# Kernel tuning notes

Measured on AMD Instinct MI355X. Metric: run time of the kernel, lower is better.

Reference implementation:

```python
import jax, jax.numpy as jnp
import numpy as np

KS = 3      # kernel_size
PAD = 1     # padding
STRIDE = 1
B, C_IN, C_OUT, H, W = 4, 64, 128, 128, 128


def _conv(x, w, stride, padding):
    return jax.lax.conv_general_dilated(
        x, w, (stride, stride), padding,
        dimension_numbers=("NCHW", "OIHW", "NCHW"))


def setup_inputs() -> dict:
    key = jax.random.key(0)
    k1, k2, k3, k4 = jax.random.split(key, 4)
    N = KS * KS
    x = jax.random.normal(k1, (B, C_IN, H, W), jnp.float32)
    # offset conv: Conv2d(inc, 2*ks*ks, 3, padding=1, stride=1). (Original inits
    # weight to 0; we use small random weights so the bilinear gather is exercised.)
    w_off = jax.random.normal(k2, (2 * N, C_IN, 3, 3), jnp.float32) * 0.01
    b_off = jax.random.normal(k3, (2 * N,), jnp.float32) * 0.01
    # main conv: Conv2d(inc, outc, ks, stride=ks, bias=False)
    w_conv = jax.random.normal(k4, (C_OUT, C_IN, KS, KS), jnp.float32) / np.sqrt(C_IN * KS * KS)
    return {"x": x, "w_off": w_off, "b_off": b_off, "w_conv": w_conv}


def deform_forward(x, w_off, b_off, w_conv):
    ks, pad, stride = KS, PAD, STRIDE
    N = ks * ks
    offset = _conv(x, w_off, stride, [(1, 1), (1, 1)]) + b_off[None, :, None, None]
    b, _, h, w = offset.shape
    xp = jnp.pad(x, ((0, 0), (0, 0), (pad, pad), (pad, pad)))
    Hp, Wp = xp.shape[2], xp.shape[3]

    # p_n: relative kernel offsets, layout [y coords (N), x coords (N)]
    r = jnp.arange(-(ks - 1) // 2, (ks - 1) // 2 + 1)
    pny, pnx = jnp.meshgrid(r, r, indexing="ij")
    p_n = jnp.concatenate([pny.ravel(), pnx.ravel()]).astype(offset.dtype).reshape(1, 2 * N, 1, 1)

    # p_0: absolute output-pixel centers (1-based due to zero padding)
    p0y, p0x = jnp.meshgrid(jnp.arange(1, h * stride + 1, stride),
                            jnp.arange(1, w * stride + 1, stride), indexing="ij")
    p_0 = jnp.concatenate([jnp.tile(p0y[None, None], (1, N, 1, 1)),
                           jnp.tile(p0x[None, None], (1, N, 1, 1))], axis=1).astype(offset.dtype)

    p = (p_0 + p_n + offset).transpose(0, 2, 3, 1)  # (b, h, w, 2N)

    # four integer corners (indices are non-differentiable / detached)
    q_lt_f = jnp.floor(jax.lax.stop_gradient(p))
    q_rb_f = q_lt_f + 1

    def clamp_yx(q):
        return jnp.concatenate([jnp.clip(q[..., :N], 0, Hp - 1),
                                jnp.clip(q[..., N:], 0, Wp - 1)], axis=-1).astype(jnp.int32)

    q_lt = clamp_yx(q_lt_f)
    q_rb = clamp_yx(q_rb_f)
    q_lb = jnp.concatenate([q_lt[..., :N], q_rb[..., N:]], axis=-1)
    q_rt = jnp.concatenate([q_rb[..., :N], q_lt[..., N:]], axis=-1)

    # points falling in the padding region snap to floor(p)
    mask = jnp.concatenate([
        (p[..., :N] < pad) | (p[..., :N] > Hp - 1 - pad),
        (p[..., N:] < pad) | (p[..., N:] > Wp - 1 - pad)], axis=-1).astype(p.dtype)
    mask = jax.lax.stop_gradient(mask)
    floor_p = jnp.floor(p)
    p = p * (1 - mask) + floor_p * mask
    p = jnp.concatenate([jnp.clip(p[..., :N], 0, Hp - 1),
                         jnp.clip(p[..., N:], 0, Wp - 1)], axis=-1)

    f = lambda q: q.astype(p.dtype)
    g_lt = (1 + (f(q_lt[..., :N]) - p[..., :N])) * (1 + (f(q_lt[..., N:]) - p[..., N:]))
    g_rb = (1 - (f(q_rb[..., :N]) - p[..., :N])) * (1 - (f(q_rb[..., N:]) - p[..., N:]))
    g_lb = (1 + (f(q_lb[..., :N]) - p[..., :N])) * (1 - (f(q_lb[..., N:]) - p[..., N:]))
    g_rt = (1 - (f(q_rt[..., :N]) - p[..., :N])) * (1 + (f(q_rt[..., N:]) - p[..., N:]))

    c = xp.shape[1]
    x_flat = xp.reshape(b, c, Hp * Wp)  # (b, c, Hp*Wp)

    def get_x_q(q):
        idx = (q[..., :N] * Wp + q[..., N:]).reshape(b, 1, h * w * N)
        return jnp.take_along_axis(x_flat, idx, axis=2).reshape(b, c, h, w, N)

    x_off = (g_lt[:, None] * get_x_q(q_lt) + g_rb[:, None] * get_x_q(q_rb)
             + g_lb[:, None] * get_x_q(q_lb) + g_rt[:, None] * get_x_q(q_rt))

    # (b, c, h, w, N=ks*ks) -> (b, c, h*ks, w*ks): sample n maps to kernel cell (n//ks, n%ks)
    x_off = x_off.reshape(b, c, h, w, ks, ks).transpose(0, 1, 2, 4, 3, 5).reshape(b, c, h * ks, w * ks)

    return _conv(x_off, w_conv, ks, "VALID")  # stride=ks, no bias


def reference(x, w_off, b_off, w_conv):
    return deform_forward(x, w_off, b_off, w_conv)
```

## Files before the change

### kernel.cpp

```cpp
#include <hip/hip_runtime.h>
#include <hip/hip_fp16.h>

#define NB 4
#define CI 64
#define CO 128
#define HH 128
#define WW 128
#define HWSZ (HH*WW)
#define TOTPX (NB*HWSZ)
#define NN 9

using half8 = __attribute__((ext_vector_type(8))) _Float16;
using f32x4 = __attribute__((ext_vector_type(4))) float;
using f32x2 = __attribute__((ext_vector_type(2))) float;

__global__ __launch_bounds__(256) void k_prep_w(const float* __restrict__ w,
                                                unsigned short* __restrict__ waF,
                                                const float* __restrict__ w_off,
                                                float* __restrict__ wP) {
    int t = blockIdx.x * 256 + threadIdx.x;
    if (t < CO * 576) {
        int oc = t / 576, r = t - oc * 576;
        int c = r / 9, n = r - c * 9;
        int i = oc >> 4, col = oc & 15;
        int ks = c >> 5, koct = (c >> 3) & 3, e = c & 7;
        int lane = koct * 16 + col;
        waF[(n * 16 + i * 2 + ks) * 512 + lane * 8 + e] =
            __half_as_ushort(__float2half_rn(w[t]));
    }
    if (t < 18 * 576) {
        int oc = t / 576, r = t - oc * 576;
        wP[r * 20 + oc] = w_off[t];
    }
}

__global__ __launch_bounds__(512, 8) void k_offsets(
    const float* __restrict__ x, const float* __restrict__ wP,
    const float* __restrict__ b_off, uchar4* __restrict__ dC,
    ushort4* __restrict__ dG, unsigned short* __restrict__ xT)
{
    __shared__ f32x2 sm[512 * 9];
    int bid = blockIdx.x;
    int b = bid >> 8, rem = bid & 255, y = rem >> 1, x0 = (rem & 1) << 6;
    int t = threadIdx.x;
    int pxl = t & 63;
    int g   = __builtin_amdgcn_readfirstlane(t >> 6);
    int xg = x0 + pxl;

    f32x2 a2[9];
    #pragma unroll
    for (int i = 0; i < 9; i++) a2[i] = {0.f, 0.f};

    #pragma unroll 2
    for (int ci = 0; ci < 8; ci++) {
        int cg = g * 8 + ci;
        const float* xpl = x + (size_t)(b * CI + cg) * HWSZ;
        #pragma unroll
        for (int ky = 0; ky < 3; ky++) {
            int yy = y + ky - 1;
            if ((unsigned)yy >= 128u) continue;
            const float* xr = xpl + yy * WW;
            #pragma unroll
            for (int kx = 0; kx < 3; kx++) {
                int xx = xg + kx - 1;
                float v = ((unsigned)xx < 128u) ? xr[xx] : 0.f;
                const f32x2* wr2 = (const f32x2*)(wP + (cg * 9 + ky * 3 + kx) * 20);
                f32x2 v2 = {v, v};
                #pragma unroll
                for (int j = 0; j < 9; j++)
                    a2[j] = __builtin_elementwise_fma(v2, wr2[j], a2[j]);
            }
        }
    }

    {
        const float* xc = x + ((size_t)(b * CI + g * 8) * HH + y) * WW + xg;
        unsigned short c8[8];
        #pragma unroll
        for (int ci = 0; ci < 8; ci++)
            c8[ci] = __half_as_ushort(__float2half_rn(xc[(size_t)ci * HWSZ]));
        size_t pbase = (size_t)((b * HH + y) * WW + xg) * 64 + g * 8;
        *(uint4*)(xT + pbase) = *(const uint4*)&c8[0];
    }

    #pragma unroll
    for (int i = 0; i < 9; i++) sm[t * 9 + i] = a2[i];
    __syncthreads();

    for (int task = t; task < 576; task += 512) {
        int p2 = task & 63, n = task >> 6;
        float ay = b_off[n], ax = b_off[9 + n];
        int jy = n >> 1, cy = n & 1;
        int jx = (9 + n) >> 1, cx = (9 + n) & 1;
        #pragma unroll
        for (int gg = 0; gg < 8; gg++) {
            ay += sm[(gg * 64 + p2) * 9 + jy][cy];
            ax += sm[(gg * 64 + p2) * 9 + jx][cx];
        }
        float py  = (float)(y + (n / 3)) + ay;
        float pxc = (float)(x0 + p2 + (n % 3)) + ax;
        float fy = floorf(py), fx = floorf(pxc);
        if (py  < 1.f || py  > 128.f) py  = fy;
        if (pxc < 1.f || pxc > 128.f) pxc = fx;
        py  = fminf(fmaxf(py,  0.f), 129.f);
        pxc = fminf(fmaxf(pxc, 0.f), 129.f);

        fy = floorf(py); fx = floorf(pxc);
        int y0 = (int)fy, x0i = (int)fx;
        int y1 = min(y0 + 1, 129), x1 = min(x0i + 1, 129);
        float wyl = 1.f + (fy - py);
        float wyr = 1.f - ((float)y1 - py);
        float wxl = 1.f + (fx - pxc);
        float wxr = 1.f - ((float)x1 - pxc);
        float glt = wyl * wxl, grb = wyr * wxr, glb = wyl * wxr, grt = wyr * wxl;
        if ((unsigned)(y0  - 1) >= 128u) { glt = 0.f; glb = 0.f; }
        if ((unsigned)(y1  - 1) >= 128u) { grb = 0.f; grt = 0.f; }
        if ((unsigned)(x0i - 1) >= 128u) { glt = 0.f; grt = 0.f; }
        if ((unsigned)(x1  - 1) >= 128u) { grb = 0.f; glb = 0.f; }

        uchar4 cu;
        cu.x = (unsigned char)min(max(y0  - 1, 0), 127);
        cu.y = (unsigned char)min(max(y1  - 1, 0), 127);
        cu.z = (unsigned char)min(max(x0i - 1, 0), 127);
        cu.w = (unsigned char)min(max(x1  - 1, 0), 127);
        ushort4 gu;
        gu.x = __half_as_ushort(__float2half_rn(glt));
        gu.y = __half_as_ushort(__float2half_rn(grb));
        gu.z = __half_as_ushort(__float2half_rn(glb));
        gu.w = __half_as_ushort(__float2half_rn(grt));
        int pixIdx = (b * HH + y) * WW + x0 + p2;
        dC[n * TOTPX + pixIdx] = cu;
        dG[n * TOTPX + pixIdx] = gu;
    }
}

__global__ __launch_bounds__(256, 4) void k_main(
    const unsigned short* __restrict__ xT, const unsigned short* __restrict__ waF,
    const uchar4* __restrict__ dC, const ushort4* __restrict__ dG,
    float* __restrict__ out)
{
    __shared__ __align__(16) unsigned short Wl[2][8192];
    __shared__ __align__(16) unsigned short Rd[4][1024];

    int bid0 = blockIdx.x;
    int bid  = ((bid0 & 7) << 7) | (bid0 >> 3);
    int b = bid >> 8, rem = bid & 255, y = rem >> 1, x0 = (rem & 1) << 6;

    int t = threadIdx.x, lane = t & 63, wv = t >> 6;
    int col = lane & 15, koct = lane >> 4;
    int gp = lane >> 2, gq = lane & 3;
    int qo = gq * 8;
    int pixG = (b * HH + y) * WW + x0 + wv * 16 + gp;
    const unsigned short* xb = xT + (size_t)b * (HWSZ * 64);

    half8 raw[8];
    f32x4 acc[8];
    #pragma unroll
    for (int i = 0; i < 8; i++) acc[i] = {0.f, 0.f, 0.f, 0.f};

    auto stage = [&](int kc, int buf) {
        #pragma unroll
        for (int p = 0; p < 4; p++) {
            const unsigned short* gsrc = waF + kc * 8192 + wv * 512 + p * 2048 + lane * 8;
            __builtin_amdgcn_global_load_lds(
                (const __attribute__((address_space(1))) unsigned int*)gsrc,
                (__attribute__((address_space(3))) unsigned int*)&Wl[buf][wv * 512 + p * 2048],
                16, 0, 0);
        }
    };
    auto issue = [&](uchar4 cu) {
        int o00 = (((int)cu.x * WW) + (int)cu.z) << 6;
        int o11 = (((int)cu.y * WW) + (int)cu.w) << 6;
        int o01 = (((int)cu.x * WW) + (int)cu.w) << 6;
        int o10 = (((int)cu.y * WW) + (int)cu.z) << 6;
        raw[0] = *(const half8*)(xb + o00 + qo);
        raw[1] = *(const half8*)(xb + o11 + qo);
        raw[2] = *(const half8*)(xb + o01 + qo);
        raw[3] = *(const half8*)(xb + o10 + qo);
        raw[4] = *(const half8*)(xb + o00 + qo + 32);
        raw[5] = *(const half8*)(xb + o11 + qo + 32);
        raw[6] = *(const half8*)(xb + o01 + qo + 32);
        raw[7] = *(const half8*)(xb + o10 + qo + 32);
    };
    auto combine_store = [&](ushort4 gu) {
        __half2 q0 = __half2half2(__ushort_as_half(gu.x));
        __half2 q1 = __half2half2(__ushort_as_half(gu.y));
        __half2 q2 = __half2half2(__ushort_as_half(gu.z));
        __half2 q3 = __half2half2(__ushort_as_half(gu.w));
        #pragma unroll
        for (int ks = 0; ks < 2; ks++) {
            __half2 vm[4];
            #pragma unroll
            for (int m = 0; m < 4; m++) {
                __half2 v = __hmul2(((const __half2*)&raw[ks * 4 + 0])[m], q0);
                v = __hfma2(((const __half2*)&raw[ks * 4 + 1])[m], q1, v);
                v = __hfma2(((const __half2*)&raw[ks * 4 + 2])[m], q2, v);
                v = __hfma2(((const __half2*)&raw[ks * 4 + 3])[m], q3, v);
                vm[m] = v;
            }
            int gz = (4 * ks + gq) ^ (gp & 7);
            *(uint4*)(&Rd[wv][0] + gp * 64 + gz * 8) = *(const uint4*)vm;
        }
    };

    stage(0, 0);
    __builtin_amdgcn_sched_barrier(0);
    uchar4  cuA = dC[pixG];          ushort4 guA = dG[pixG];
    uchar4  cuB = dC[TOTPX + pixG];  ushort4 guB = dG[TOTPX + pixG];
    __builtin_amdgcn_sched_barrier(0);
    issue(cuA);
    __builtin_amdgcn_sched_barrier(0);
    asm volatile("s_waitcnt vmcnt(8)" ::: "memory");
    __builtin_amdgcn_s_barrier();
    __builtin_amdgcn_sched_barrier(0);

#define ITER(KC)                                                              \
  {                                                                           \
    if ((KC) < 8) stage((KC) + 1, ((KC) & 1) ^ 1);                            \
    __builtin_amdgcn_sched_barrier(0);                                        \
    uchar4 cuN; ushort4 guN;                                                  \
    if ((KC) < 7) { cuN = dC[((KC)+2) * TOTPX + pixG];                        \
                    guN = dG[((KC)+2) * TOTPX + pixG]; }                      \
    __builtin_amdgcn_sched_barrier(0);                                        \
    combine_store(guA);                                                       \
    asm volatile("s_waitcnt lgkmcnt(0)" ::: "memory");                        \
    __builtin_amdgcn_sched_barrier(0);                                        \
    half8 bfr[2];                                                             \
    _Pragma("unroll")                                                         \
    for (int ks = 0; ks < 2; ks++) {                                          \
      int gz = (4 * ks + koct) ^ (col & 7);                                   \
      bfr[ks] = *(const half8*)(&Rd[wv][0] + col * 64 + gz * 8);              \
    }                                                                         \
    __builtin_amdgcn_sched_barrier(0);                                        \
    if ((KC) < 8) issue(cuB);                                                 \
    __builtin_amdgcn_sched_barrier(0);                                        \
    __builtin_amdgcn_s_setprio(1);                                            \
    { const unsigned short* wl = &Wl[(KC) & 1][0];                            \
      _Pragma("unroll")                                                       \
      for (int ks = 0; ks < 2; ks++)                                          \
        _Pragma("unroll")                                                     \
        for (int i = 0; i < 8; i++) {                                         \
          half8 af = *(const half8*)(wl + (i * 2 + ks) * 512 + lane * 8);     \
          acc[i] = __builtin_amdgcn_mfma_f32_16x16x32_f16(af, bfr[ks],        \
                                                          acc[i], 0, 0, 0); } } \
    __builtin_amdgcn_s_setprio(0);                                            \
    if ((KC) < 8) {                                                           \
      if ((KC) < 7) asm volatile("s_waitcnt vmcnt(10)" ::: "memory");         \
      else          asm volatile("s_waitcnt vmcnt(8)"  ::: "memory");         \
      __builtin_amdgcn_s_barrier();                                           \
      __builtin_amdgcn_sched_barrier(0);                                      \
    }                                                                         \
    cuA = cuB; guA = guB;                                                     \
    cuB = ((KC) < 7) ? cuN : cuB; guB = ((KC) < 7) ? guN : guB;               \
  }

    ITER(0) ITER(1) ITER(2) ITER(3) ITER(4) ITER(5) ITER(6) ITER(7) ITER(8)
#undef ITER

    int ob0 = b * CO * HWSZ + y * WW + x0 + wv * 16 + col;
    #pragma unroll
    for (int i = 0; i < 8; i++)
        #pragma unroll
        for (int r = 0; r < 4; r++) {
            int oc = i * 16 + koct * 4 + r;
            out[ob0 + oc * HWSZ] = acc[i][r];
        }
}

extern "C" void kernel_launch(void* const* d_in, const int* in_sizes, int n_in,
                              void* d_out, int out_size, void* d_ws, size_t ws_size,
                              hipStream_t stream) {
    const float* x      = (const float*)d_in[0];
    const float* w_off  = (const float*)d_in[1];
    const float* b_off  = (const float*)d_in[2];
    const float* w_conv = (const float*)d_in[3];
    float* out = (float*)d_out;

    char* wsb = (char*)d_ws;
    unsigned short* xT  = (unsigned short*)wsb;
    uchar4*         dC  = (uchar4*)(wsb + (size_t)TOTPX * 64 * 2);
    ushort4*        dG  = (ushort4*)(wsb + (size_t)TOTPX * 64 * 2 + (size_t)NN * TOTPX * 4);
    unsigned short* waF = (unsigned short*)(wsb + (size_t)TOTPX * 64 * 2
                                            + (size_t)NN * TOTPX * 4 + (size_t)NN * TOTPX * 8);
    float*          wP  = (float*)(wsb + (size_t)TOTPX * 64 * 2
                                   + (size_t)NN * TOTPX * 4 + (size_t)NN * TOTPX * 8
                                   + (size_t)CO * 576 * 2);

    k_prep_w<<<(CO * 576 + 255) / 256, 256, 0, stream>>>(w_conv, waF, w_off, wP);
    k_offsets<<<1024, 512, 0, stream>>>(x, wP, b_off, dC, dG, xT);
    k_main<<<1024, 256, 0, stream>>>(xT, waF, dC, dG, out);
}
```

Baseline: 58.39 us.

## Fuse offset computation into main deformable conv kernel, split NHWC transpose

The offset convolution and bilinear-coefficient computation now run inside the main MFMA kernel, one block per image row of 128 pixels and 512 threads. Coordinates and weights stay in LDS rather than going to global dC/dG arrays. The fp16 NHWC transpose of x moves to a separate LDS-tiled kernel, because the fused kernel gathers neighbouring pixels from other rows and so needs the whole transposed image first. This removes the global round-trip for offsets but adds a launch, halves the block count to 512, and makes the MFMA phase wait on the scalar offset conv inside each block.

```diff
diff --git a/kernel.cpp b/kernel.cpp
--- a/kernel.cpp
+++ b/kernel.cpp
@@ -34,71 +34,91 @@
     }
 }
 
-__global__ __launch_bounds__(512, 8) void k_offsets(
-    const float* __restrict__ x, const float* __restrict__ wP,
-    const float* __restrict__ b_off, uchar4* __restrict__ dC,
-    ushort4* __restrict__ dG, unsigned short* __restrict__ xT)
-{
-    __shared__ f32x2 sm[512 * 9];
+__global__ __launch_bounds__(256) void k_nhwc(const float* __restrict__ x,
+                                              unsigned short* __restrict__ xT) {
+    __shared__ float tl[64 * 65];
     int bid = blockIdx.x;
     int b = bid >> 8, rem = bid & 255, y = rem >> 1, x0 = (rem & 1) << 6;
     int t = threadIdx.x;
-    int pxl = t & 63;
-    int g   = __builtin_amdgcn_readfirstlane(t >> 6);
-    int xg = x0 + pxl;
-
-    f32x2 a2[9];
-    #pragma unroll
-    for (int i = 0; i < 9; i++) a2[i] = {0.f, 0.f};
-
-    #pragma unroll 2
-    for (int ci = 0; ci < 8; ci++) {
-        int cg = g * 8 + ci;
-        const float* xpl = x + (size_t)(b * CI + cg) * HWSZ;
-        #pragma unroll
-        for (int ky = 0; ky < 3; ky++) {
-            int yy = y + ky - 1;
-            if ((unsigned)yy >= 128u) continue;
-            const float* xr = xpl + yy * WW;
+    #pragma unroll
+    for (int i = 0; i < 16; i++) {
+        int idx = t + i * 256;
+        int c = idx >> 6, xl = idx & 63;
+        tl[c * 65 + xl] = x[((size_t)(b * CI + c) * HH + y) * WW + x0 + xl];
+    }
+    __syncthreads();
+    #pragma unroll
+    for (int i = 0; i < 16; i++) {
+        int idx = t + i * 256;
+        int xl = idx >> 6, c = idx & 63;
+        xT[(size_t)((b * HH + y) * WW + x0 + xl) * 64 + c] =
+            __half_as_ushort(__float2half_rn(tl[c * 65 + xl]));
+    }
+}
+
+__global__ __launch_bounds__(512, 4) void k_fused(
+    const float* __restrict__ x, const unsigned short* __restrict__ xT,
+    const unsigned short* __restrict__ waF, const float* __restrict__ wP,
+    const float* __restrict__ b_off, float* __restrict__ out)
+{
+    __shared__ __align__(16) char LB[62976];
+    f32x2*          sm  = (f32x2*)LB;
+    unsigned short* WlA = (unsigned short*)LB;
+    unsigned short* WlB = (unsigned short*)(LB + 16384);
+    unsigned short* Rd  = (unsigned short*)(LB + 32768);
+    uchar4*         dCl = (uchar4*)(LB + 49152);
+    ushort4*        dGl = (ushort4*)(LB + 49152 + 4608);
+
+    int bid0 = blockIdx.x;
+    int bid  = ((bid0 & 7) << 6) | (bid0 >> 3);
+    int b = bid >> 7, y = bid & 127;
+    int t = threadIdx.x;
+
+    {
+        int px = t & 127;
+        int g  = __builtin_amdgcn_readfirstlane(t >> 7);
+        f32x2 a2[9];
+        #pragma unroll
+        for (int i = 0; i < 9; i++) a2[i] = {0.f, 0.f};
+
+        #pragma unroll 2
+        for (int ci = 0; ci < 16; ci++) {
+            int cg = g * 16 + ci;
+            const float* xpl = x + (size_t)(b * CI + cg) * HWSZ;
             #pragma unroll
-            for (int kx = 0; kx < 3; kx++) {
-                int xx = xg + kx - 1;
-                float v = ((unsigned)xx < 128u) ? xr[xx] : 0.f;
-                const f32x2* wr2 = (const f32x2*)(wP + (cg * 9 + ky * 3 + kx) * 20);
-                f32x2 v2 = {v, v};
+            for (int ky = 0; ky < 3; ky++) {
+                int yy = y + ky - 1;
+                if ((unsigned)yy >= 128u) continue;
+                const float* xr = xpl + yy * WW;
                 #pragma unroll
-                for (int j = 0; j < 9; j++)
-                    a2[j] = __builtin_elementwise_fma(v2, wr2[j], a2[j]);
+                for (int kx = 0; kx < 3; kx++) {
+                    int xx = px + kx - 1;
+                    float v = ((unsigned)xx < 128u) ? xr[xx] : 0.f;
+                    const f32x2* wr2 = (const f32x2*)(wP + (cg * 9 + ky * 3 + kx) * 20);
+                    f32x2 v2 = {v, v};
+                    #pragma unroll
+                    for (int j = 0; j < 9; j++)
+                        a2[j] = __builtin_elementwise_fma(v2, wr2[j], a2[j]);
+                }
             }
         }
-    }
-
-    {
-        const float* xc = x + ((size_t)(b * CI + g * 8) * HH + y) * WW + xg;
-        unsigned short c8[8];
-        #pragma unroll
-        for (int ci = 0; ci < 8; ci++)
-            c8[ci] = __half_as_ushort(__float2half_rn(xc[(size_t)ci * HWSZ]));
-        size_t pbase = (size_t)((b * HH + y) * WW + xg) * 64 + g * 8;
-        *(uint4*)(xT + pbase) = *(const uint4*)&c8[0];
-    }
-
-    #pragma unroll
-    for (int i = 0; i < 9; i++) sm[t * 9 + i] = a2[i];
+        #pragma unroll
+        for (int i = 0; i < 9; i++) sm[t * 9 + i] = a2[i];
+    }
     __syncthreads();
 
-    for (int task = t; task < 576; task += 512) {
-        int p2 = task & 63, n = task >> 6;
+    for (int task = t; task < 1152; task += 512) {
+        int p2 = task & 127, n = task >> 7;
         float ay = b_off[n], ax = b_off[9 + n];
         int jy = n >> 1, cy = n & 1;
         int jx = (9 + n) >> 1, cx = (9 + n) & 1;
         #pragma unroll
-        for (int gg = 0; gg < 8; gg++) {
-            ay += sm[(gg * 64 + p2) * 9 + jy][cy];
-            ax += sm[(gg * 64 + p2) * 9 + jx][cx];
+        for (int gg = 0; gg < 4; gg++) {
+            ay += sm[(gg * 128 + p2) * 9 + jy][cy];
+            ax += sm[(gg * 128 + p2) * 9 + jx][cx];
         }
         float py  = (float)(y + (n / 3)) + ay;
-        float pxc = (float)(x0 + p2 + (n % 3)) + ax;
+        float pxc = (float)(p2 + (n % 3)) + ax;
         float fy = floorf(py), fx = floorf(pxc);
         if (py  < 1.f || py  > 128.f) py  = fy;
         if (pxc < 1.f || pxc > 128.f) pxc = fx;
@@ -128,43 +148,31 @@
         gu.y = __half_as_ushort(__float2half_rn(grb));
         gu.z = __half_as_ushort(__float2half_rn(glb));
         gu.w = __half_as_ushort(__float2half_rn(grt));
-        int pixIdx = (b * HH + y) * WW + x0 + p2;
-        dC[n * TOTPX + pixIdx] = cu;
-        dG[n * TOTPX + pixIdx] = gu;
-    }
-}
-
-__global__ __launch_bounds__(256, 4) void k_main(
-    const unsigned short* __restrict__ xT, const unsigned short* __restrict__ waF,
-    const uchar4* __restrict__ dC, const ushort4* __restrict__ dG,
-    float* __restrict__ out)
-{
-    __shared__ __align__(16) unsigned short Wl[2][8192];
-    __shared__ __align__(16) unsigned short Rd[4][1024];
-
-    int bid0 = blockIdx.x;
-    int bid  = ((bid0 & 7) << 7) | (bid0 >> 3);
-    int b = bid >> 8, rem = bid & 255, y = rem >> 1, x0 = (rem & 1) << 6;
-
-    int t = threadIdx.x, lane = t & 63, wv = t >> 6;
+        dCl[n * 128 + p2] = cu;
+        dGl[n * 128 + p2] = gu;
+    }
+    __syncthreads();
+
+    int lane = t & 63, wv = t >> 6;
     int col = lane & 15, koct = lane >> 4;
     int gp = lane >> 2, gq = lane & 3;
     int qo = gq * 8;
-    int pixG = (b * HH + y) * WW + x0 + wv * 16 + gp;
+    int pxG = wv * 16 + gp;
     const unsigned short* xb = xT + (size_t)b * (HWSZ * 64);
+    unsigned short* Rdw = Rd + wv * 1024;
 
     half8 raw[8];
     f32x4 acc[8];
     #pragma unroll
     for (int i = 0; i < 8; i++) acc[i] = {0.f, 0.f, 0.f, 0.f};
 
-    auto stage = [&](int kc, int buf) {
-        #pragma unroll
-        for (int p = 0; p < 4; p++) {
-            const unsigned short* gsrc = waF + kc * 8192 + wv * 512 + p * 2048 + lane * 8;
+    auto stage = [&](int kc, unsigned short* buf) {
+        #pragma unroll
+        for (int p = 0; p < 2; p++) {
+            const unsigned short* gsrc = waF + kc * 8192 + wv * 1024 + p * 512 + lane * 8;
             __builtin_amdgcn_global_load_lds(
                 (const __attribute__((address_space(1))) unsigned int*)gsrc,
-                (__attribute__((address_space(3))) unsigned int*)&Wl[buf][wv * 512 + p * 2048],
+                (__attribute__((address_space(3))) unsigned int*)(buf + wv * 1024 + p * 512),
                 16, 0, 0);
         }
     };
@@ -199,14 +207,14 @@
                 vm[m] = v;
             }
             int gz = (4 * ks + gq) ^ (gp & 7);
-            *(uint4*)(&Rd[wv][0] + gp * 64 + gz * 8) = *(const uint4*)vm;
+            *(uint4*)(Rdw + gp * 64 + gz * 8) = *(const uint4*)vm;
         }
     };
 
-    stage(0, 0);
-    __builtin_amdgcn_sched_barrier(0);
-    uchar4  cuA = dC[pixG];          ushort4 guA = dG[pixG];
-    uchar4  cuB = dC[TOTPX + pixG];  ushort4 guB = dG[TOTPX + pixG];
+    stage(0, WlA);
+    __builtin_amdgcn_sched_barrier(0);
+    uchar4  cuA = dCl[pxG];        ushort4 guA = dGl[pxG];
+    uchar4  cuB = dCl[128 + pxG];  ushort4 guB = dGl[128 + pxG];
     __builtin_amdgcn_sched_barrier(0);
     issue(cuA);
     __builtin_amdgcn_sched_barrier(0);
@@ -216,11 +224,11 @@
 
 #define ITER(KC)                                                              \
   {                                                                           \
-    if ((KC) < 8) stage((KC) + 1, ((KC) & 1) ^ 1);                            \
+    if ((KC) < 8) stage((KC) + 1, ((KC) & 1) ? WlA : WlB);                    \
     __builtin_amdgcn_sched_barrier(0);                                        \
     uchar4 cuN; ushort4 guN;                                                  \
-    if ((KC) < 7) { cuN = dC[((KC)+2) * TOTPX + pixG];                        \
-                    guN = dG[((KC)+2) * TOTPX + pixG]; }                      \
+    if ((KC) < 7) { cuN = dCl[((KC)+2) * 128 + pxG];                          \
+                    guN = dGl[((KC)+2) * 128 + pxG]; }                        \
     __builtin_amdgcn_sched_barrier(0);                                        \
     combine_store(guA);                                                       \
     asm volatile("s_waitcnt lgkmcnt(0)" ::: "memory");                        \
@@ -229,13 +237,13 @@
     _Pragma("unroll")                                                         \
     for (int ks = 0; ks < 2; ks++) {                                          \
       int gz = (4 * ks + koct) ^ (col & 7);                                   \
-      bfr[ks] = *(const half8*)(&Rd[wv][0] + col * 64 + gz * 8);              \
+      bfr[ks] = *(const half8*)(Rdw + col * 64 + gz * 8);                     \
     }                                                                         \
     __builtin_amdgcn_sched_barrier(0);                                        \
     if ((KC) < 8) issue(cuB);                                                 \
     __builtin_amdgcn_sched_barrier(0);                                        \
     __builtin_amdgcn_s_setprio(1);                                            \
-    { const unsigned short* wl = &Wl[(KC) & 1][0];                            \
+    { const unsigned short* wl = ((KC) & 1) ? WlB : WlA;                      \
       _Pragma("unroll")                                                       \
       for (int ks = 0; ks < 2; ks++)                                          \
         _Pragma("unroll")                                                     \
@@ -245,8 +253,7 @@
                                                           acc[i], 0, 0, 0); } } \
     __builtin_amdgcn_s_setprio(0);                                            \
     if ((KC) < 8) {                                                           \
-      if ((KC) < 7) asm volatile("s_waitcnt vmcnt(10)" ::: "memory");         \
-      else          asm volatile("s_waitcnt vmcnt(8)"  ::: "memory");         \
+      asm volatile("s_waitcnt vmcnt(8)" ::: "memory");                        \
       __builtin_amdgcn_s_barrier();                                           \
       __builtin_amdgcn_sched_barrier(0);                                      \
     }                                                                         \
@@ -257,7 +264,7 @@
     ITER(0) ITER(1) ITER(2) ITER(3) ITER(4) ITER(5) ITER(6) ITER(7) ITER(8)
 #undef ITER
 
-    int ob0 = b * CO * HWSZ + y * WW + x0 + wv * 16 + col;
+    int ob0 = b * CO * HWSZ + y * WW + wv * 16 + col;
     #pragma unroll
     for (int i = 0; i < 8; i++)
         #pragma unroll
@@ -278,15 +285,10 @@
 
     char* wsb = (char*)d_ws;
     unsigned short* xT  = (unsigned short*)wsb;
-    uchar4*         dC  = (uchar4*)(wsb + (size_t)TOTPX * 64 * 2);
-    ushort4*        dG  = (ushort4*)(wsb + (size_t)TOTPX * 64 * 2 + (size_t)NN * TOTPX * 4);
-    unsigned short* waF = (unsigned short*)(wsb + (size_t)TOTPX * 64 * 2
-                                            + (size_t)NN * TOTPX * 4 + (size_t)NN * TOTPX * 8);
-    float*          wP  = (float*)(wsb + (size_t)TOTPX * 64 * 2
-                                   + (size_t)NN * TOTPX * 4 + (size_t)NN * TOTPX * 8
-                                   + (size_t)CO * 576 * 2);
+    unsigned short* waF = (unsigned short*)(wsb + (size_t)TOTPX * 64 * 2);
+    float*          wP  = (float*)(wsb + (size_t)TOTPX * 64 * 2 + (size_t)CO * 576 * 2);
 
     k_prep_w<<<(CO * 576 + 255) / 256, 256, 0, stream>>>(w_conv, waF, w_off, wP);
-    k_offsets<<<1024, 512, 0, stream>>>(x, wP, b_off, dC, dG, xT);
-    k_main<<<1024, 256, 0, stream>>>(xT, waF, dC, dG, out);
-}
+    k_nhwc<<<1024, 256, 0, stream>>>(x, xT);
+    k_fused<<<512, 512, 0, stream>>>(x, xT, waF, wP, b_off, out);
+}
```

Measured after the change: 59.76 us. +2.4%, slower.
